# Performance work log

Measured on AMD Instinct MI355X. Metric: run time of the kernel, lower is better.

## Reference

```python
import jax, jax.numpy as jnp
import numpy as np

EPS = 1e-7  # K.epsilon()
N_ROUTINGS = 3


def squash(v, axis=-1):
    s2 = jnp.sum(jnp.square(v), axis=axis, keepdims=True)
    scale = s2 / (1.0 + s2) / jnp.sqrt(s2 + EPS)
    return scale * v


def setup_inputs() -> dict:
    key = jax.random.key(0)
    k1, k2 = jax.random.split(key)
    B, IN_CAPS, IN_DIM = 128, 1152, 8
    N_CAPS, DIM = 32, 16
    inputs = jax.random.normal(k1, (B, IN_CAPS, IN_DIM), dtype=jnp.float32)
    # glorot-uniform-ish scale for W [n_capsule, in_caps, dim_capsule, in_dim]
    limit = np.sqrt(6.0 / (IN_DIM + DIM)).astype(np.float32)
    W = jax.random.uniform(k2, (N_CAPS, IN_CAPS, DIM, IN_DIM), dtype=jnp.float32,
                           minval=-limit, maxval=limit)
    return {"inputs": inputs, "W": W}


def reference(inputs, W):
    # inputs: [b, i, l]; W: [j, i, k, l] -> u_hat: [b, j, i, k]
    u_hat = jnp.einsum('jikl,bil->bjik', W, inputs)
    b = jnp.zeros(u_hat.shape[:3], dtype=u_hat.dtype)  # [b, j, i]
    v = None
    for r in range(N_ROUTINGS):
        c = jax.nn.softmax(b, axis=1)                 # softmax over output caps j
        s = jnp.einsum('bji,bjik->bjk', c, u_hat)     # weighted sum over input caps i
        v = squash(s, axis=-1)                        # [b, j, k]
        if r < N_ROUTINGS - 1:
            b = b + jnp.einsum('bjik,bjk->bji', u_hat, v)  # agreement
    return v
```

## Files before the change

kernel.cpp:

```cpp
#include <hip/hip_runtime.h>
#include <hip/hip_bf16.h>
#include <stdint.h>


using fab = __attribute__((ext_vector_type(8))) short;
using fcc = __attribute__((ext_vector_type(4))) float;

__device__ __forceinline__ uint32_t bfr(float f) {
    uint32_t u = __float_as_uint(f);
    return (u + 0x7fffu + ((u >> 16) & 1u)) >> 16;
}

__global__ __launch_bounds__(256)
void prep_w(const float* __restrict__ W, ushort* __restrict__ W3)
{
    const int t = blockIdx.x * 256 + threadIdx.x;
    const int k = t & 15, j = (t >> 4) & 31, i = t >> 9;
    const float* src = W + (((size_t)j * 1152 + i) * 16 + k) * 8;
    const float4 a = *reinterpret_cast<const float4*>(src);
    const float4 b = *reinterpret_cast<const float4*>(src + 4);
    uint4 o;
    o.x = bfr(a.x) | (bfr(a.y) << 16);
    o.y = bfr(a.z) | (bfr(a.w) << 16);
    o.z = bfr(b.x) | (bfr(b.y) << 16);
    o.w = bfr(b.z) | (bfr(b.w) << 16);
    *reinterpret_cast<uint4*>(W3 + (size_t)t * 8) = o;
}

__global__ __launch_bounds__(256)
void prep_x(const float* __restrict__ x, ushort* __restrict__ X2)
{
    const int t = blockIdx.x * 256 + threadIdx.x;
    const int b = t & 127, i = t >> 7;
    const float* src = x + ((size_t)b * 1152 + i) * 8;
    const float4 a = *reinterpret_cast<const float4*>(src);
    const float4 bb = *reinterpret_cast<const float4*>(src + 4);
    uint4 o;
    o.x = bfr(a.x) | (bfr(a.y) << 16);
    o.y = bfr(a.z) | (bfr(a.w) << 16);
    o.z = bfr(bb.x) | (bfr(bb.y) << 16);
    o.w = bfr(bb.z) | (bfr(bb.w) << 16);
    *reinterpret_cast<uint4*>(X2 + (size_t)t * 8) = o;
}

template<int R>
__global__ __launch_bounds__(512)
void caps_route_mfma(const ushort* __restrict__ W3,
                     const ushort* __restrict__ X2,
                     const float* __restrict__ Vacc,
                     float* __restrict__ s)
{
    __shared__ float pl[2][8][16];
    __shared__ float tr[8][1024];

    const int tid  = threadIdx.x;
    const int lane = tid & 63;
    const int w    = tid >> 6;
    const int bl   = lane & 15;
    const int kg   = lane >> 4;
    const bool lo  = (kg == 0);
    const int bg   = blockIdx.x >> 6;
    const int sl   = blockIdx.x & 63;
    const int i0   = sl * 18;
    const int b0   = bg * 16;

    fab zf;
    #pragma unroll
    for (int q = 0; q < 8; ++q) zf[q] = 0;

    auto loadA = [&](int i, int t) -> fab {
        return lo ? *reinterpret_cast<const fab*>(
                        W3 + (((size_t)i * 32 + w * 4 + t) * 16 + bl) * 8)
                  : zf;
    };
    auto loadB = [&](int i) -> fab {
        return lo ? *reinterpret_cast<const fab*>(
                        X2 + ((size_t)i * 128 + b0 + bl) * 8)
                  : zf;
    };

    float Vr[4][4];
    if (R > 0) {
        #pragma unroll
        for (int t = 0; t < 4; ++t)
            #pragma unroll
            for (int r = 0; r < 4; ++r)
                Vr[t][r] = Vacc[((size_t)(b0 + bl) * 32 + w * 4 + t) * 16
                                + kg * 4 + r] * 1.44269504f;
    }

    fcc sacc[4];
    #pragma unroll
    for (int t = 0; t < 4; ++t)
        #pragma unroll
        for (int r = 0; r < 4; ++r) sacc[t][r] = 0.0f;

    auto body = [&](const fab* A, const fab& B, int ii) {
        const fcc cz = {0.0f, 0.0f, 0.0f, 0.0f};
        fcc u[4];
        #pragma unroll
        for (int t = 0; t < 4; ++t)
            u[t] = __builtin_amdgcn_mfma_f32_16x16x32_bf16(A[t], B, cz, 0, 0, 0);

        float cf4[4];
        if (R == 0) {
            #pragma unroll
            for (int t = 0; t < 4; ++t) cf4[t] = 0.03125f;
        } else {
            float e[4];
            float ps = 0.0f;
            #pragma unroll
            for (int t = 0; t < 4; ++t) {
                float p = u[t][0] * Vr[t][0];
                p = fmaf(u[t][1], Vr[t][1], p);
                p = fmaf(u[t][2], Vr[t][2], p);
                p = fmaf(u[t][3], Vr[t][3], p);
                p += __shfl_xor(p, 16);
                p += __shfl_xor(p, 32);
                e[t] = exp2f(p);
                ps += e[t];
            }
            const int ib = ii & 1;
            if (lane < 16) pl[ib][w][bl] = ps;
            __syncthreads();
            float den = pl[ib][0][bl];
            #pragma unroll
            for (int ww = 1; ww < 8; ++ww) den += pl[ib][ww][bl];
            const float inv = __builtin_amdgcn_rcpf(den);
            #pragma unroll
            for (int t = 0; t < 4; ++t) cf4[t] = e[t] * inv;
        }
        #pragma unroll
        for (int t = 0; t < 4; ++t)
            #pragma unroll
            for (int r = 0; r < 4; ++r)
                sacc[t][r] = fmaf(cf4[t], u[t][r], sacc[t][r]);
    };

    fab A0[4], A1[4], B0, B1;
    #pragma unroll
    for (int t = 0; t < 4; ++t) A0[t] = loadA(i0, t);
    B0 = loadB(i0);

    for (int ii = 0; ii < 18; ii += 2) {
        {
            const int ip = i0 + ii + 1;
            #pragma unroll
            for (int t = 0; t < 4; ++t) A1[t] = loadA(ip, t);
            B1 = loadB(ip);
        }
        body(A0, B0, ii);
        {
            int ip = i0 + ii + 2;
            if (ip > 1151) ip = 1151;
            #pragma unroll
            for (int t = 0; t < 4; ++t) A0[t] = loadA(ip, t);
            B0 = loadB(ip);
        }
        body(A1, B1, ii + 1);
    }

    {
        float* ep = &tr[w][0];
        #pragma unroll
        for (int t = 0; t < 4; ++t)
            #pragma unroll
            for (int r = 0; r < 4; ++r) {
                const int off = t * 16 + kg * 4 + r;
                ep[off * 16 + (bl ^ (off & 15))] = sacc[t][r];
            }
        float* sg = s + (size_t)b0 * 512 + w * 64;
        #pragma unroll
        for (int c = 0; c < 16; ++c) {
            const float v = ep[lane * 16 + (c ^ (lane & 15))];
            atomicAdd(&sg[(size_t)c * 512 + lane], v);
        }
    }
}

#define WJ        (1152 * 128)
#define I_TILE_F  24
#define NSLICE_F  48

template<int R>
__global__ __launch_bounds__(256)
void caps_route_f32(const float* __restrict__ x,
                    const float* __restrict__ W,
                    const float* __restrict__ Vacc,
                    float* __restrict__ s)
{
    __shared__ float Wt[2][4096];
    __shared__ float xs[8 * 192];

    const int tid  = threadIdx.x;
    const int lane = tid & 63;
    const int wv   = tid >> 6;
    const int j    = lane & 31;
    const int kh   = lane >> 5;
    const int bg   = blockIdx.x / NSLICE_F;
    const int sl   = blockIdx.x % NSLICE_F;
    const int i0   = sl * I_TILE_F;
    const int b0   = bg * 8 + wv * 2;

    const float* wsrc[4];
    #pragma unroll
    for (int t = 0; t < 4; ++t) {
        const int q  = (wv * 4 + t) * 1024 + lane * 16;
        const int rr = q >> 8;
        const int cb = (q & 255) ^ ((rr & 15) << 4);
        const int js = rr & 31;
        const int c  = (rr >> 5) * 64 + (cb >> 2);
        wsrc[t] = W + (size_t)js * WJ + c;
    }

    auto stage = [&](int buf, int i) {
        #pragma unroll
        for (int t = 0; t < 4; ++t)
            __builtin_amdgcn_global_load_lds(
                (const __attribute__((address_space(1))) uint32_t*)
                    (wsrc[t] + (size_t)i * 128),
                (__attribute__((address_space(3))) uint32_t*)
                    &Wt[buf][(wv * 4 + t) * 256], 16, 0, 0);
    };

    stage(0, i0);

    for (int cf = tid; cf < 384; cf += 256) {
        const int bl = cf / 48;
        const int rm = cf - bl * 48;
        float4 v = *reinterpret_cast<const float4*>(
            x + ((size_t)(bg * 8 + bl) * 1152 + i0) * 8 + rm * 4);
        *reinterpret_cast<float4*>(xs + bl * 192 + rm * 4) = v;
    }

    float Vr[2][8];
    if (R > 0) {
        #pragma unroll
        for (int bb = 0; bb < 2; ++bb) {
            const float* vp = Vacc + ((size_t)(b0 + bb) * 32 + j) * 16 + kh * 8;
            const float4 va = *reinterpret_cast<const float4*>(vp);
            const float4 vb = *reinterpret_cast<const float4*>(vp + 4);
            Vr[bb][0] = va.x * 1.44269504f; Vr[bb][1] = va.y * 1.44269504f;
            Vr[bb][2] = va.z * 1.44269504f; Vr[bb][3] = va.w * 1.44269504f;
            Vr[bb][4] = vb.x * 1.44269504f; Vr[bb][5] = vb.y * 1.44269504f;
            Vr[bb][6] = vb.z * 1.44269504f; Vr[bb][7] = vb.w * 1.44269504f;
        }
    }

    float sacc[2][8];
    #pragma unroll
    for (int bb = 0; bb < 2; ++bb)
        #pragma unroll
        for (int kk = 0; kk < 8; ++kk) sacc[bb][kk] = 0.0f;

    __syncthreads();

    const int sw = (j & 15) << 4;

    for (int ii = 0; ii < I_TILE_F; ++ii) {
        const int cur = ii & 1;
        if (ii + 1 < I_TILE_F) stage(cur ^ 1, i0 + ii + 1);

        float4 xa[2], xb[2];
        #pragma unroll
        for (int bb = 0; bb < 2; ++bb) {
            const float* xp = xs + (wv * 2 + bb) * 192 + ii * 8;
            xa[bb] = *reinterpret_cast<const float4*>(xp);
            xb[bb] = *reinterpret_cast<const float4*>(xp + 4);
        }

        const char* lbase = reinterpret_cast<const char*>(&Wt[cur][0]) + lane * 256;

        float u[2][8];
        #pragma unroll
        for (int kk = 0; kk < 8; ++kk) {
            const float4 w0 = *reinterpret_cast<const float4*>(lbase + ((kk * 32) ^ sw));
            const float4 w1 = *reinterpret_cast<const float4*>(lbase + ((kk * 32 + 16) ^ sw));
            #pragma unroll
            for (int bb = 0; bb < 2; ++bb) {
                float acc;
                acc = w0.x * xa[bb].x;
                acc = fmaf(w0.y, xa[bb].y, acc);
                acc = fmaf(w0.z, xa[bb].z, acc);
                acc = fmaf(w0.w, xa[bb].w, acc);
                acc = fmaf(w1.x, xb[bb].x, acc);
                acc = fmaf(w1.y, xb[bb].y, acc);
                acc = fmaf(w1.z, xb[bb].z, acc);
                acc = fmaf(w1.w, xb[bb].w, acc);
                u[bb][kk] = acc;
            }
        }

        if (R == 0) {
            #pragma unroll
            for (int bb = 0; bb < 2; ++bb)
                #pragma unroll
                for (int kk = 0; kk < 8; ++kk)
                    sacc[bb][kk] = fmaf(0.03125f, u[bb][kk], sacc[bb][kk]);
        } else {
            float p0 = u[0][0] * Vr[0][0];
            float p1 = u[1][0] * Vr[1][0];
            #pragma unroll
            for (int kk = 1; kk < 8; ++kk) {
                p0 = fmaf(u[0][kk], Vr[0][kk], p0);
                p1 = fmaf(u[1][kk], Vr[1][kk], p1);
            }
            p0 += __shfl_xor(p0, 32);
            p1 += __shfl_xor(p1, 32);
            const float pq = kh ? p1 : p0;
            const float e  = exp2f(pq);
            float den = e;
            den += __shfl_xor(den, 1);
            den += __shfl_xor(den, 2);
            den += __shfl_xor(den, 4);
            den += __shfl_xor(den, 8);
            den += __shfl_xor(den, 16);
            const float cf_own = e * __builtin_amdgcn_rcpf(den);
            const float cf_oth = __shfl_xor(cf_own, 32);
            const float cf0 = kh ? cf_oth : cf_own;
            const float cf1 = kh ? cf_own : cf_oth;
            #pragma unroll
            for (int kk = 0; kk < 8; ++kk) {
                sacc[0][kk] = fmaf(cf0, u[0][kk], sacc[0][kk]);
                sacc[1][kk] = fmaf(cf1, u[1][kk], sacc[1][kk]);
            }
        }
        __syncthreads();
    }

    {
        float* ep = &Wt[0][0] + wv * 1024;
        #pragma unroll
        for (int bb = 0; bb < 2; ++bb)
            #pragma unroll
            for (int kk = 0; kk < 8; ++kk)
                ep[bb * 512 + j * 16 + ((kh * 8 + kk) ^ ((j >> 1) & 15))] =
                    sacc[bb][kk];

        float* sg = s + (size_t)b0 * 512;
        #pragma unroll
        for (int c = 0; c < 16; ++c) {
            const int m   = c * 64 + lane;
            const int bb2 = m >> 9;
            const int j2  = (m >> 4) & 31;
            const int k2  = m & 15;
            const float v = ep[bb2 * 512 + j2 * 16 + (k2 ^ ((j2 >> 1) & 15))];
            atomicAdd(&sg[m], v);
        }
    }
}

template<int MODE>
__global__ __launch_bounds__(256)
void caps_squash(float* __restrict__ s,
                 float* __restrict__ Vacc,
                 float* __restrict__ out)
{
    const int t = blockIdx.x * 256 + threadIdx.x;
    const float sv = s[t];
    float p = sv * sv;
    p += __shfl_xor(p, 1);
    p += __shfl_xor(p, 2);
    p += __shfl_xor(p, 4);
    p += __shfl_xor(p, 8);
    const float scale = p / ((1.0f + p) * sqrtf(p + 1e-7f));
    const float v = scale * sv;
    if (MODE == 0)      { Vacc[t] = v;  s[t] = 0.0f; }
    else if (MODE == 1) { Vacc[t] += v; s[t] = 0.0f; }
    else                { out[t] = v; }
}

extern "C" void kernel_launch(void* const* d_in, const int* in_sizes, int n_in,
                              void* d_out, int out_size, void* d_ws, size_t ws_size,
                              hipStream_t stream)
{
    const float* x = (const float*)d_in[0];
    const float* W = (const float*)d_in[1];
    float* out = (float*)d_out;

    const size_t W3B = (size_t)589824 * 16;
    const size_t X2B = (size_t)147456 * 16;
    const size_t SB  = (size_t)65536 * sizeof(float);

    if (ws_size >= W3B + X2B + 2 * SB) {
        ushort* W3  = (ushort*)d_ws;
        ushort* X2  = (ushort*)((char*)d_ws + W3B);
        float* Vacc = (float*)((char*)d_ws + W3B + X2B);
        float* sbuf = Vacc + 65536;

        prep_w<<<2304, 256, 0, stream>>>(W, (ushort*)W3);
        prep_x<<<576, 256, 0, stream>>>(x, (ushort*)X2);
        hipMemsetAsync(sbuf, 0, SB, stream);

        dim3 grid(512);
        dim3 blk(512);
        caps_route_mfma<0><<<grid, blk, 0, stream>>>(W3, X2, Vacc, sbuf);
        caps_squash<0><<<256, 256, 0, stream>>>(sbuf, Vacc, out);
        caps_route_mfma<1><<<grid, blk, 0, stream>>>(W3, X2, Vacc, sbuf);
        caps_squash<1><<<256, 256, 0, stream>>>(sbuf, Vacc, out);
        caps_route_mfma<2><<<grid, blk, 0, stream>>>(W3, X2, Vacc, sbuf);
        caps_squash<2><<<256, 256, 0, stream>>>(sbuf, Vacc, out);
    } else {
        float* Vacc = (float*)d_ws;
        float* sbuf = Vacc + 65536;
        hipMemsetAsync(sbuf, 0, SB, stream);

        dim3 grid(16 * NSLICE_F);
        dim3 blk(256);
        caps_route_f32<0><<<grid, blk, 0, stream>>>(x, W, Vacc, sbuf);
        caps_squash<0><<<256, 256, 0, stream>>>(sbuf, Vacc, out);
        caps_route_f32<1><<<grid, blk, 0, stream>>>(x, W, Vacc, sbuf);
        caps_squash<1><<<256, 256, 0, stream>>>(sbuf, Vacc, out);
        caps_route_f32<2><<<grid, blk, 0, stream>>>(x, W, Vacc, sbuf);
        caps_squash<2><<<256, 256, 0, stream>>>(sbuf, Vacc, out);
    }
}
```

Before: 115.7 us.

## Fuse squash into routing kernel via last-block counter and drop memset

The separate squash kernels are removed. The last block to finish each batch group, found through an atomic counter, squashes the accumulated s, writes Vacc or the output, and re-zeroes s. The memset of s and the counters is folded into prep_x. This removes three kernel launches and a memset, at the cost of a thread fence and an atomic per block plus a serialized tail done by one block per batch group.

```diff
diff --git a/kernel.cpp b/kernel.cpp
--- a/kernel.cpp
+++ b/kernel.cpp
@@ -28,7 +28,8 @@
 }
 
 __global__ __launch_bounds__(256)
-void prep_x(const float* __restrict__ x, ushort* __restrict__ X2)
+void prep_x(const float* __restrict__ x, ushort* __restrict__ X2,
+            float4* __restrict__ s4, uint32_t* __restrict__ cnt)
 {
     const int t = blockIdx.x * 256 + threadIdx.x;
     const int b = t & 127, i = t >> 7;
@@ -41,17 +42,24 @@
     o.z = bfr(bb.x) | (bfr(bb.y) << 16);
     o.w = bfr(bb.z) | (bfr(bb.w) << 16);
     *reinterpret_cast<uint4*>(X2 + (size_t)t * 8) = o;
+
+    if (t < 16384) s4[t] = make_float4(0.f, 0.f, 0.f, 0.f);
+    if (t < 24) cnt[t] = 0u;
 }
 
 template<int R>
 __global__ __launch_bounds__(512)
 void caps_route_mfma(const ushort* __restrict__ W3,
                      const ushort* __restrict__ X2,
-                     const float* __restrict__ Vacc,
-                     float* __restrict__ s)
+                     const float* Vacc,
+                     float* VaccW,
+                     float* s,
+                     float* __restrict__ out,
+                     uint32_t* __restrict__ cnt)
 {
     __shared__ float pl[2][8][16];
     __shared__ float tr[8][1024];
+    __shared__ int lastf;
 
     const int tid  = threadIdx.x;
     const int lane = tid & 63;
@@ -174,6 +182,42 @@
         for (int c = 0; c < 16; ++c) {
             const float v = ep[lane * 16 + (c ^ (lane & 15))];
             atomicAdd(&sg[(size_t)c * 512 + lane], v);
+        }
+    }
+
+    __threadfence();
+    __syncthreads();
+    if (tid == 0) {
+        const uint32_t old = atomicAdd(&cnt[R * 8 + bg], 1u);
+        lastf = (old == 63);
+    }
+    __syncthreads();
+    if (lastf) {
+        __threadfence();
+        const int bb = tid >> 5;
+        const int jj = tid & 31;
+        float* srow = s + ((size_t)(b0 + bb) * 32 + jj) * 16;
+        float vv[16];
+        float p = 0.0f;
+        #pragma unroll
+        for (int k = 0; k < 16; ++k) {
+            vv[k] = __hip_atomic_load(&srow[k], __ATOMIC_RELAXED,
+                                      __HIP_MEMORY_SCOPE_AGENT);
+            p = fmaf(vv[k], vv[k], p);
+        }
+        const float scale = p / ((1.0f + p) * sqrtf(p + 1e-7f));
+        if (R == 2) {
+            float* orow = out + ((size_t)(b0 + bb) * 32 + jj) * 16;
+            #pragma unroll
+            for (int k = 0; k < 16; ++k) orow[k] = scale * vv[k];
+        } else {
+            float* vrow = VaccW + ((size_t)(b0 + bb) * 32 + jj) * 16;
+            #pragma unroll
+            for (int k = 0; k < 16; ++k) {
+                const float nv = scale * vv[k];
+                vrow[k] = (R == 0) ? nv : (vrow[k] + nv);
+                srow[k] = 0.0f;
+            }
         }
     }
 }
@@ -382,24 +426,21 @@
     const size_t X2B = (size_t)147456 * 16;
     const size_t SB  = (size_t)65536 * sizeof(float);
 
-    if (ws_size >= W3B + X2B + 2 * SB) {
-        ushort* W3  = (ushort*)d_ws;
-        ushort* X2  = (ushort*)((char*)d_ws + W3B);
-        float* Vacc = (float*)((char*)d_ws + W3B + X2B);
-        float* sbuf = Vacc + 65536;
-
-        prep_w<<<2304, 256, 0, stream>>>(W, (ushort*)W3);
-        prep_x<<<576, 256, 0, stream>>>(x, (ushort*)X2);
-        hipMemsetAsync(sbuf, 0, SB, stream);
+    if (ws_size >= W3B + X2B + 2 * SB + 4096) {
+        ushort* W3    = (ushort*)d_ws;
+        ushort* X2    = (ushort*)((char*)d_ws + W3B);
+        float* Vacc   = (float*)((char*)d_ws + W3B + X2B);
+        float* sbuf   = Vacc + 65536;
+        uint32_t* cnt = (uint32_t*)((char*)d_ws + W3B + X2B + 2 * SB);
+
+        prep_w<<<2304, 256, 0, stream>>>(W, W3);
+        prep_x<<<576, 256, 0, stream>>>(x, X2, (float4*)sbuf, cnt);
 
         dim3 grid(512);
         dim3 blk(512);
-        caps_route_mfma<0><<<grid, blk, 0, stream>>>(W3, X2, Vacc, sbuf);
-        caps_squash<0><<<256, 256, 0, stream>>>(sbuf, Vacc, out);
-        caps_route_mfma<1><<<grid, blk, 0, stream>>>(W3, X2, Vacc, sbuf);
-        caps_squash<1><<<256, 256, 0, stream>>>(sbuf, Vacc, out);
-        caps_route_mfma<2><<<grid, blk, 0, stream>>>(W3, X2, Vacc, sbuf);
-        caps_squash<2><<<256, 256, 0, stream>>>(sbuf, Vacc, out);
+        caps_route_mfma<0><<<grid, blk, 0, stream>>>(W3, X2, Vacc, Vacc, sbuf, out, cnt);
+        caps_route_mfma<1><<<grid, blk, 0, stream>>>(W3, X2, Vacc, Vacc, sbuf, out, cnt);
+        caps_route_mfma<2><<<grid, blk, 0, stream>>>(W3, X2, Vacc, Vacc, sbuf, out, cnt);
     } else {
         float* Vacc = (float*)d_ws;
         float* sbuf = Vacc + 65536;
```

Result: slower. 354.3 us (+206.2%).

## Fold squash into routing kernels and merge prep kernels

Applied to the files above, without the earlier changes.

Removes the two intermediate squash kernels by having each routing pass recompute the squashed v from the raw s buffers of earlier iterations (s0, s1) with cross-lane shuffles. Separate output buffers per iteration replace the in-place Vacc/s reset, so one memset covers all three. The two bf16 conversion kernels are merged into a single launch. This cuts kernel launches and global round-trips at the cost of some redundant squash arithmetic in every block.

```diff
diff --git a/kernel.cpp b/kernel.cpp
--- a/kernel.cpp
+++ b/kernel.cpp
@@ -12,43 +12,43 @@
 }
 
 __global__ __launch_bounds__(256)
-void prep_w(const float* __restrict__ W, ushort* __restrict__ W3)
+void prep(const float* __restrict__ W, const float* __restrict__ x,
+          ushort* __restrict__ W3, ushort* __restrict__ X2)
 {
     const int t = blockIdx.x * 256 + threadIdx.x;
-    const int k = t & 15, j = (t >> 4) & 31, i = t >> 9;
-    const float* src = W + (((size_t)j * 1152 + i) * 16 + k) * 8;
-    const float4 a = *reinterpret_cast<const float4*>(src);
-    const float4 b = *reinterpret_cast<const float4*>(src + 4);
-    uint4 o;
-    o.x = bfr(a.x) | (bfr(a.y) << 16);
-    o.y = bfr(a.z) | (bfr(a.w) << 16);
-    o.z = bfr(b.x) | (bfr(b.y) << 16);
-    o.w = bfr(b.z) | (bfr(b.w) << 16);
-    *reinterpret_cast<uint4*>(W3 + (size_t)t * 8) = o;
-}
-
-__global__ __launch_bounds__(256)
-void prep_x(const float* __restrict__ x, ushort* __restrict__ X2)
-{
-    const int t = blockIdx.x * 256 + threadIdx.x;
-    const int b = t & 127, i = t >> 7;
-    const float* src = x + ((size_t)b * 1152 + i) * 8;
-    const float4 a = *reinterpret_cast<const float4*>(src);
-    const float4 bb = *reinterpret_cast<const float4*>(src + 4);
-    uint4 o;
-    o.x = bfr(a.x) | (bfr(a.y) << 16);
-    o.y = bfr(a.z) | (bfr(a.w) << 16);
-    o.z = bfr(bb.x) | (bfr(bb.y) << 16);
-    o.w = bfr(bb.z) | (bfr(bb.w) << 16);
-    *reinterpret_cast<uint4*>(X2 + (size_t)t * 8) = o;
+    {
+        const int k = t & 15, j = (t >> 4) & 31, i = t >> 9;
+        const float* src = W + (((size_t)j * 1152 + i) * 16 + k) * 8;
+        const float4 a = *reinterpret_cast<const float4*>(src);
+        const float4 b = *reinterpret_cast<const float4*>(src + 4);
+        uint4 o;
+        o.x = bfr(a.x) | (bfr(a.y) << 16);
+        o.y = bfr(a.z) | (bfr(a.w) << 16);
+        o.z = bfr(b.x) | (bfr(b.y) << 16);
+        o.w = bfr(b.z) | (bfr(b.w) << 16);
+        *reinterpret_cast<uint4*>(W3 + (size_t)t * 8) = o;
+    }
+    if (t < 147456) {
+        const int b = t & 127, i = t >> 7;
+        const float* src = x + ((size_t)b * 1152 + i) * 8;
+        const float4 a = *reinterpret_cast<const float4*>(src);
+        const float4 bb = *reinterpret_cast<const float4*>(src + 4);
+        uint4 o;
+        o.x = bfr(a.x) | (bfr(a.y) << 16);
+        o.y = bfr(a.z) | (bfr(a.w) << 16);
+        o.z = bfr(bb.x) | (bfr(bb.y) << 16);
+        o.w = bfr(bb.z) | (bfr(bb.w) << 16);
+        *reinterpret_cast<uint4*>(X2 + (size_t)t * 8) = o;
+    }
 }
 
 template<int R>
 __global__ __launch_bounds__(512)
 void caps_route_mfma(const ushort* __restrict__ W3,
                      const ushort* __restrict__ X2,
-                     const float* __restrict__ Vacc,
-                     float* __restrict__ s)
+                     const float* __restrict__ s0,
+                     const float* __restrict__ s1,
+                     float* __restrict__ sout)
 {
     __shared__ float pl[2][8][16];
     __shared__ float tr[8][1024];
@@ -82,11 +82,26 @@
     float Vr[4][4];
     if (R > 0) {
         #pragma unroll
-        for (int t = 0; t < 4; ++t)
-            #pragma unroll
-            for (int r = 0; r < 4; ++r)
-                Vr[t][r] = Vacc[((size_t)(b0 + bl) * 32 + w * 4 + t) * 16
-                                + kg * 4 + r] * 1.44269504f;
+        for (int t = 0; t < 4; ++t) {
+            const size_t ro = ((size_t)(b0 + bl) * 32 + w * 4 + t) * 16 + kg * 4;
+            const float4 a = *reinterpret_cast<const float4*>(s0 + ro);
+            float q = a.x * a.x + a.y * a.y + a.z * a.z + a.w * a.w;
+            q += __shfl_xor(q, 16);
+            q += __shfl_xor(q, 32);
+            const float sc = q / ((1.0f + q) * sqrtf(q + 1e-7f)) * 1.44269504f;
+            Vr[t][0] = a.x * sc; Vr[t][1] = a.y * sc;
+            Vr[t][2] = a.z * sc; Vr[t][3] = a.w * sc;
+            if (R == 2) {
+                const float4 b = *reinterpret_cast<const float4*>(s1 + ro);
+                float q1 = b.x * b.x + b.y * b.y + b.z * b.z + b.w * b.w;
+                q1 += __shfl_xor(q1, 16);
+                q1 += __shfl_xor(q1, 32);
+                const float sc1 =
+                    q1 / ((1.0f + q1) * sqrtf(q1 + 1e-7f)) * 1.44269504f;
+                Vr[t][0] += b.x * sc1; Vr[t][1] += b.y * sc1;
+                Vr[t][2] += b.z * sc1; Vr[t][3] += b.w * sc1;
+            }
+        }
     }
 
     fcc sacc[4];
@@ -169,13 +184,27 @@
                 const int off = t * 16 + kg * 4 + r;
                 ep[off * 16 + (bl ^ (off & 15))] = sacc[t][r];
             }
-        float* sg = s + (size_t)b0 * 512 + w * 64;
+        float* sg = sout + (size_t)b0 * 512 + w * 64;
         #pragma unroll
         for (int c = 0; c < 16; ++c) {
             const float v = ep[lane * 16 + (c ^ (lane & 15))];
             atomicAdd(&sg[(size_t)c * 512 + lane], v);
         }
     }
+}
+
+__global__ __launch_bounds__(256)
+void caps_squash_out(const float* __restrict__ s2, float* __restrict__ out)
+{
+    const int t = blockIdx.x * 256 + threadIdx.x;
+    const float sv = s2[t];
+    float p = sv * sv;
+    p += __shfl_xor(p, 1);
+    p += __shfl_xor(p, 2);
+    p += __shfl_xor(p, 4);
+    p += __shfl_xor(p, 8);
+    const float scale = p / ((1.0f + p) * sqrtf(p + 1e-7f));
+    out[t] = scale * sv;
 }
 
 #define WJ        (1152 * 128)
@@ -382,24 +411,22 @@
     const size_t X2B = (size_t)147456 * 16;
     const size_t SB  = (size_t)65536 * sizeof(float);
 
-    if (ws_size >= W3B + X2B + 2 * SB) {
-        ushort* W3  = (ushort*)d_ws;
-        ushort* X2  = (ushort*)((char*)d_ws + W3B);
-        float* Vacc = (float*)((char*)d_ws + W3B + X2B);
-        float* sbuf = Vacc + 65536;
-
-        prep_w<<<2304, 256, 0, stream>>>(W, (ushort*)W3);
-        prep_x<<<576, 256, 0, stream>>>(x, (ushort*)X2);
-        hipMemsetAsync(sbuf, 0, SB, stream);
+    if (ws_size >= W3B + X2B + 3 * SB) {
+        ushort* W3 = (ushort*)d_ws;
+        ushort* X2 = (ushort*)((char*)d_ws + W3B);
+        float* s0  = (float*)((char*)d_ws + W3B + X2B);
+        float* s1  = s0 + 65536;
+        float* s2  = s1 + 65536;
+
+        hipMemsetAsync(s0, 0, 3 * SB, stream);
+        prep<<<2304, 256, 0, stream>>>(W, x, W3, X2);
 
         dim3 grid(512);
         dim3 blk(512);
-        caps_route_mfma<0><<<grid, blk, 0, stream>>>(W3, X2, Vacc, sbuf);
-        caps_squash<0><<<256, 256, 0, stream>>>(sbuf, Vacc, out);
-        caps_route_mfma<1><<<grid, blk, 0, stream>>>(W3, X2, Vacc, sbuf);
-        caps_squash<1><<<256, 256, 0, stream>>>(sbuf, Vacc, out);
-        caps_route_mfma<2><<<grid, blk, 0, stream>>>(W3, X2, Vacc, sbuf);
-        caps_squash<2><<<256, 256, 0, stream>>>(sbuf, Vacc, out);
+        caps_route_mfma<0><<<grid, blk, 0, stream>>>(W3, X2, s0, s0, s0);
+        caps_route_mfma<1><<<grid, blk, 0, stream>>>(W3, X2, s0, s0, s1);
+        caps_route_mfma<2><<<grid, blk, 0, stream>>>(W3, X2, s0, s1, s2);
+        caps_squash_out<<<256, 256, 0, stream>>>(s2, out);
     } else {
         float* Vacc = (float*)d_ws;
         float* sbuf = Vacc + 65536;
```

Measured after the change: 114.4 us. No clear change (-1.1%).
